# Kernel tuning notes

Measured on AMD Instinct MI355X. Metric: run time of the kernel, lower is better.

Reference implementation:

```python
import jax, jax.numpy as jnp
import numpy as np

V, D, L = 256, 512, 12
B, S = 8, 8192
EPS = 1e-5


def layernorm(x, g, b):
    mu = jnp.mean(x, axis=-1, keepdims=True)
    var = jnp.var(x, axis=-1, keepdims=True)
    return (x - mu) * jax.lax.rsqrt(var + EPS) * g + b


def log_g(x):
    # log of g(x) = x+0.5 if x>=0 else sigmoid(x)
    return jnp.where(x >= 0, jnp.log(jax.nn.relu(x) + 0.5), -jax.nn.softplus(-x))


def heinsen_scan_log(log_coeffs, log_values):
    # h_t = a_t * h_{t-1} + b_t in log-space, parallel over seq (axis=1)
    a_star = jnp.cumsum(log_coeffs, axis=1)
    log_h0_plus_b = jax.lax.cumlogsumexp(log_values - a_star, axis=1)
    return jnp.exp(a_star + log_h0_plus_b)


def min_gru(x, W):
    hg = x @ W                      # [B,S,2D]
    hidden, gate = hg[..., :D], hg[..., D:]
    log_coeffs = -jax.nn.softplus(gate)      # log(1 - z)
    log_z = -jax.nn.softplus(-gate)          # log z
    log_values = log_z + log_g(hidden)
    return heinsen_scan_log(log_coeffs, log_values)


def setup_inputs() -> dict:
    key = jax.random.key(0)
    k0, k1, k2 = jax.random.split(key, 3)
    tokens = jax.random.randint(k0, (B, S), 0, V)
    emb = jax.random.normal(k1, (V, D), dtype=jnp.float32) * 0.02
    # xavier uniform for Linear(D, 2D): fan_in=D, fan_out=2D
    lim = float(np.sqrt(6.0 / (D + 2 * D)))
    W = jax.random.uniform(k2, (L, D, 2 * D), minval=-lim, maxval=lim, dtype=jnp.float32)
    return {
        "tokens": tokens,
        "emb": emb,
        "ln_g": jnp.ones((L, D), jnp.float32),
        "ln_b": jnp.zeros((L, D), jnp.float32),
        "W": W,
        "norm_g": jnp.ones((D,), jnp.float32),
        "norm_b": jnp.zeros((D,), jnp.float32),
    }


def reference(tokens, emb, ln_g, ln_b, W, norm_g, norm_b):
    x = emb[tokens]                 # [B,S,D]
    for i in range(L):
        h = layernorm(x, ln_g[i], ln_b[i])
        x = x + min_gru(h, W[i])
    x = layernorm(x, norm_g, norm_b)
    logits = x @ emb.T              # tied lm_head, [B,S,V]
    return logits
```

## Files before the change

### kernel.cpp

```cpp
#include <hip/hip_runtime.h>
#include <stdint.h>

#define D 512
#define VOCAB 256
#define NLAYER 12
#define BB 8
#define SS 8192
#define CH 128
#define SL 64

typedef __bf16 bf16x8 __attribute__((ext_vector_type(8)));
typedef float f32x4 __attribute__((ext_vector_type(4)));
typedef _Float16 half2_t __attribute__((ext_vector_type(2)));

__device__ __forceinline__ unsigned short f2bf(float f) {
  union { float f; uint32_t u; } c; c.f = f;
  uint32_t u = c.u;
  u += 0x7FFFu + ((u >> 16) & 1u);
  return (unsigned short)(u >> 16);
}

__device__ __forceinline__ void st_f32(float* p, float v) { *p = v; }
__device__ __forceinline__ void st_f32(unsigned short* p, float v) { *p = f2bf(v); }

__device__ __forceinline__ float rcpf_(float x) { return __builtin_amdgcn_rcpf(x); }

__device__ __forceinline__ uint32_t pack_fv(float f, float v) {
  union { half2_t h; uint32_t u; } c;
  c.h.x = (_Float16)f;
  c.h.y = (_Float16)v;
  return c.u;
}

__device__ __forceinline__ void unpack_fv(uint32_t u, float& f, float& v) {
  union { uint32_t u; half2_t h; } c; c.u = u;
  f = (float)c.h.x;
  v = (float)c.h.y;
}

__device__ __forceinline__ void gl_lds16(const unsigned short* g, unsigned short* l) {
  __builtin_amdgcn_global_load_lds((const __attribute__((address_space(1))) void*)(const void*)g,
                                   (__attribute__((address_space(3))) void*)(void*)l, 16, 0, 0);
}

__global__ __launch_bounds__(256) void k_gather(const int* __restrict__ toks,
                                                const float* __restrict__ emb,
                                                float* __restrict__ x) {
  int T = blockIdx.x * 256 + threadIdx.x;
  int row = T >> 6, lane = T & 63;
  int tok = toks[row] & (VOCAB - 1);
  const float4* s = (const float4*)(emb + (size_t)tok * D) + lane * 2;
  float4* d = (float4*)(x + (size_t)row * D) + lane * 2;
  d[0] = s[0];
  d[1] = s[1];
}

__global__ __launch_bounds__(256) void k_convW(const float* __restrict__ W,
                                               unsigned short* __restrict__ Wt) {
  __shared__ float tile[32][33];
  int bid = blockIdx.x;
  int l = bid >> 9;
  int rem = bid & 511;
  int kt = rem >> 5, nt = rem & 31;
  int k0 = kt * 32, n0 = nt * 32;
  int tx = threadIdx.x & 31, ty = threadIdx.x >> 5;
  const float* Wl = W + (size_t)l * D * 2 * D;
  for (int i = 0; i < 4; i++) {
    int k = k0 + ty + 8 * i;
    tile[ty + 8 * i][tx] = Wl[(size_t)k * 1024 + n0 + tx];
  }
  __syncthreads();
  unsigned short* Wtl = Wt + (size_t)l * 1024 * D;
  for (int i = 0; i < 4; i++) {
    int n = n0 + ty + 8 * i;
    Wtl[(size_t)n * D + k0 + tx] = f2bf(tile[tx][ty + 8 * i]);
  }
}

__global__ __launch_bounds__(256) void k_fragW(const unsigned short* __restrict__ Wt,
                                               unsigned short* __restrict__ WtF) {
  int t = blockIdx.x * 256 + threadIdx.x;
  int lane = t & 63;
  int tile = t >> 6;
  int l = tile >> 10;
  int rem = tile & 1023;
  int n16 = rem >> 4, kt = rem & 15;
  const unsigned short* src = Wt + (size_t)l * 1024 * 512 +
                              (size_t)(n16 * 16 + (lane & 15)) * 512 + kt * 32 + (lane >> 4) * 8;
  unsigned short* dst = WtF + (size_t)l * 1024 * 512 + ((size_t)tile * 64 + lane) * 8 -
                        (size_t)l * 1024 * 512 + (size_t)l * 1024 * 512;
  *(uint4*)(WtF + (size_t)l * 524288 + ((size_t)rem * 64 + lane) * 8) = *(const uint4*)src;
  (void)dst;
}

__global__ __launch_bounds__(256) void k_convEmb(const float* __restrict__ e,
                                                 unsigned short* __restrict__ o) {
  int t = blockIdx.x * 256 + threadIdx.x;
  const float4* s = (const float4*)e + (size_t)t * 2;
  float4 a = s[0], b = s[1];
  uint32_t w0 = (uint32_t)f2bf(a.x) | ((uint32_t)f2bf(a.y) << 16);
  uint32_t w1 = (uint32_t)f2bf(a.z) | ((uint32_t)f2bf(a.w) << 16);
  uint32_t w2 = (uint32_t)f2bf(b.x) | ((uint32_t)f2bf(b.y) << 16);
  uint32_t w3 = (uint32_t)f2bf(b.z) | ((uint32_t)f2bf(b.w) << 16);
  uint4 r; r.x = w0; r.y = w1; r.z = w2; r.w = w3;
  ((uint4*)o)[t] = r;
}

__global__ __launch_bounds__(256) void k_ln(const float* __restrict__ x,
                                            const float* __restrict__ g,
                                            const float* __restrict__ b,
                                            unsigned short* __restrict__ o) {
  int wv = threadIdx.x >> 6, lane = threadIdx.x & 63;
  size_t row = (size_t)blockIdx.x * 4 + wv;
  const float4* xr = (const float4*)(x + row * D) + lane * 2;
  float4 v0 = xr[0], v1 = xr[1];
  float s = v0.x + v0.y + v0.z + v0.w + v1.x + v1.y + v1.z + v1.w;
  float ss = v0.x * v0.x + v0.y * v0.y + v0.z * v0.z + v0.w * v0.w +
             v1.x * v1.x + v1.y * v1.y + v1.z * v1.z + v1.w * v1.w;
  for (int m = 32; m; m >>= 1) {
    s += __shfl_xor(s, m, 64);
    ss += __shfl_xor(ss, m, 64);
  }
  float mu = s * (1.0f / 512.0f);
  float var = ss * (1.0f / 512.0f) - mu * mu;
  float rstd = rsqrtf(var + 1e-5f);
  const float4* gp = (const float4*)g + lane * 2;
  const float4* bp = (const float4*)b + lane * 2;
  float4 g0 = gp[0], g1 = gp[1], b0 = bp[0], b1 = bp[1];
  uint32_t w0 = (uint32_t)f2bf((v0.x - mu) * rstd * g0.x + b0.x) |
                ((uint32_t)f2bf((v0.y - mu) * rstd * g0.y + b0.y) << 16);
  uint32_t w1 = (uint32_t)f2bf((v0.z - mu) * rstd * g0.z + b0.z) |
                ((uint32_t)f2bf((v0.w - mu) * rstd * g0.w + b0.w) << 16);
  uint32_t w2 = (uint32_t)f2bf((v1.x - mu) * rstd * g1.x + b1.x) |
                ((uint32_t)f2bf((v1.y - mu) * rstd * g1.y + b1.y) << 16);
  uint32_t w3 = (uint32_t)f2bf((v1.z - mu) * rstd * g1.z + b1.z) |
                ((uint32_t)f2bf((v1.w - mu) * rstd * g1.w + b1.w) << 16);
  uint4 r; r.x = w0; r.y = w1; r.z = w2; r.w = w3;
  ((uint4*)(o + row * D))[lane] = r;
}

__global__ __launch_bounds__(256, 2) void k_gemm_act(const unsigned short* __restrict__ A,
                                                     const unsigned short* __restrict__ Bt,
                                                     uint32_t* __restrict__ fv,
                                                     float* __restrict__ P,
                                                     float* __restrict__ Q) {
  __shared__ __align__(16) unsigned short As[64 * 512];
  const int tid = threadIdx.x;
  const int lane = tid & 63;
  const int wave = tid >> 6;
  const int m0 = blockIdx.x * 64;
  const int qm = lane & 15;
  const int hi = lane >> 4;
  for (int j = 0; j < 16; j++) {
    int r = wave * 16 + j;
    int cg = (lane & ~7) | ((lane & 7) ^ (r & 7));
    gl_lds16(A + (size_t)(m0 + r) * 512 + cg * 8, As + r * 512);
  }
  __syncthreads();

  const int b_loc = m0 >> 13;
  const int c_chunk = (m0 & (SS - 1)) >> 6;
  const size_t pq0 = ((size_t)b_loc * CH + c_chunk) * 512;

  for (int np = 0; np < 2; np++) {
    const int c0 = np * 256 + wave * 64;
    const int n16h = (c0 >> 4);
    f32x4 ah[4][4] = {};
    f32x4 ag[4][4] = {};
    bf16x8 bh[2][4], bg[2][4];
    for (int j = 0; j < 4; j++) {
      bh[0][j] = *(const bf16x8*)(Bt + (((size_t)(n16h + j) * 16 + 0) * 64 + lane) * 8);
      bg[0][j] = *(const bf16x8*)(Bt + (((size_t)(n16h + j + 32) * 16 + 0) * 64 + lane) * 8);
    }
    for (int kt = 0; kt < 16; kt++) {
      const int cur = kt & 1;
      if (kt < 15) {
        const int nxt = cur ^ 1;
        for (int j = 0; j < 4; j++) {
          bh[nxt][j] = *(const bf16x8*)(Bt + (((size_t)(n16h + j) * 16 + kt + 1) * 64 + lane) * 8);
          bg[nxt][j] = *(const bf16x8*)(Bt + (((size_t)(n16h + j + 32) * 16 + kt + 1) * 64 + lane) * 8);
        }
      }
      bf16x8 af[4];
      for (int i = 0; i < 4; i++) {
        int row = i * 16 + qm;
        int cgd = kt * 4 + hi;
        int cl = (cgd & ~7) | ((cgd & 7) ^ (row & 7));
        af[i] = *(const bf16x8*)(&As[row * 512 + cl * 8]);
      }
      for (int i = 0; i < 4; i++)
        for (int j = 0; j < 4; j++) {
          ah[i][j] = __builtin_amdgcn_mfma_f32_16x16x32_bf16(af[i], bh[cur][j], ah[i][j], 0, 0, 0);
          ag[i][j] = __builtin_amdgcn_mfma_f32_16x16x32_bf16(af[i], bg[cur][j], ag[i][j], 0, 0, 0);
        }
    }
    const int rq = hi * 4;
    for (int j = 0; j < 4; j++) {
      float cp = 1.f, cq = 0.f;
      for (int i = 0; i < 4; i++) {
        float sp = 1.f, sq = 0.f;
        for (int r = 0; r < 4; r++) {
          float h = ah[i][j][r];
          float g = ag[i][j][r];
          float e = __expf(g);
          float f = rcpf_(1.0f + e);
          float sg = 1.0f - f;
          float gf = h >= 0.0f ? h + 0.5f : rcpf_(1.0f + __expf(-h));
          float v = sg * gf;
          int rowg = m0 + i * 16 + rq + r;
          fv[(size_t)rowg * 512 + c0 + j * 16 + qm] = pack_fv(f, v);
          sp *= f;
          sq = sq * f + v;
        }
        float op = __shfl_xor(sp, 16), oq = __shfl_xor(sq, 16);
        float tp = sp * op;
        float tq = (lane & 16) ? (oq * sp + sq) : (sq * op + oq);
        op = __shfl_xor(tp, 32); oq = __shfl_xor(tq, 32);
        sp = tp * op;
        sq = (lane & 32) ? (oq * tp + tq) : (tq * op + oq);
        cq = cq * sp + sq;
        cp = cp * sp;
      }
      if (hi == 0) {
        P[pq0 + c0 + j * 16 + qm] = cp;
        Q[pq0 + c0 + j * 16 + qm] = cq;
      }
    }
  }
}

__global__ __launch_bounds__(256) void k_gemm(const unsigned short* __restrict__ A,
                                              const unsigned short* __restrict__ Bt,
                                              float* __restrict__ C, int N, int MT) {
  __shared__ __align__(16) unsigned short As[128 * 64];
  __shared__ __align__(16) unsigned short Bs[128 * 64];
  const int tid = threadIdx.x;
  const int lane = tid & 63;
  const int wave = tid >> 6;
  const int bid = blockIdx.x;
  const int mt = bid % MT;
  const int nt = bid / MT;
  const int m0 = mt * 128, n0 = nt * 128;
  const int wr = (wave >> 1) * 64;
  const int wc = (wave & 1) * 64;
  const int lrow = lane >> 3;
  const int lcs = ((lane & 7) ^ lrow) * 8;
  const unsigned short* Ag = A + (size_t)(m0 + wave * 32 + lrow) * 512 + lcs;
  const unsigned short* Bg = Bt + (size_t)(n0 + wave * 32 + lrow) * 512 + lcs;
  unsigned short* Al = As + wave * 32 * 64;
  unsigned short* Bl = Bs + wave * 32 * 64;
  const int qm = lane & 15;
  const int hi = lane >> 4;
  f32x4 acc[4][4] = {};
  for (int k0 = 0; k0 < 512; k0 += 64) {
    for (int j = 0; j < 4; j++) gl_lds16(Ag + k0 + (size_t)j * 8 * 512, Al + j * 512);
    for (int j = 0; j < 4; j++) gl_lds16(Bg + k0 + (size_t)j * 8 * 512, Bl + j * 512);
    __syncthreads();
    for (int ks = 0; ks < 2; ks++) {
      const int sw = ((ks * 4 + hi) ^ (qm & 7)) * 8;
      bf16x8 af[4], bfr[4];
      for (int i = 0; i < 4; i++) {
        af[i] = *(const bf16x8*)(&As[(wr + i * 16 + qm) * 64 + sw]);
        bfr[i] = *(const bf16x8*)(&Bs[(wc + i * 16 + qm) * 64 + sw]);
      }
      for (int i = 0; i < 4; i++)
        for (int j = 0; j < 4; j++)
          acc[i][j] = __builtin_amdgcn_mfma_f32_16x16x32_bf16(af[i], bfr[j], acc[i][j], 0, 0, 0);
    }
    __syncthreads();
  }
  const int col = lane & 15;
  const int rq = (lane >> 4) * 4;
  for (int i = 0; i < 4; i++)
    for (int j = 0; j < 4; j++)
      for (int r = 0; r < 4; r++)
        C[(size_t)(m0 + wr + i * 16 + rq + r) * N + (n0 + wc + j * 16 + col)] = acc[i][j][r];
}

__global__ __launch_bounds__(256) void k_scan2(const float* __restrict__ P,
                                               const float* __restrict__ Q,
                                               float* __restrict__ Hs) {
  int T = blockIdx.x * 256 + threadIdx.x;
  int d = T & 511;
  int b = T >> 9;
  float h = 0.f;
  for (int c = 0; c < CH; c++) {
    size_t i = ((size_t)b * CH + c) * 512 + d;
    Hs[i] = h;
    h = P[i] * h + Q[i];
  }
}

__global__ __launch_bounds__(256) void k_scan3(const uint32_t* __restrict__ fv,
                                               const float* __restrict__ Hs,
                                               float* __restrict__ x) {
  int T = blockIdx.x * 256 + threadIdx.x;
  int d = T & 511;
  int bc = T >> 9;
  int c = bc & (CH - 1);
  int b = bc >> 7;
  const uint32_t* base = fv + ((size_t)b * SS + c * SL) * 512 + d;
  float* xb = x + ((size_t)b * SS + c * SL) * 512 + d;
  float h = Hs[T];
  for (int s = 0; s < SL; s++) {
    float f, v;
    unpack_fv(base[(size_t)s * 512], f, v);
    h = f * h + v;
    xb[(size_t)s * 512] += h;
  }
}

extern "C" void kernel_launch(void* const* d_in, const int* in_sizes, int n_in,
                              void* d_out, int out_size, void* d_ws, size_t ws_size,
                              hipStream_t stream) {
  const int* toks = (const int*)d_in[0];
  const float* emb = (const float*)d_in[1];
  const float* ln_g = (const float*)d_in[2];
  const float* ln_b = (const float*)d_in[3];
  const float* W = (const float*)d_in[4];
  const float* norm_g = (const float*)d_in[5];
  const float* norm_b = (const float*)d_in[6];
  float* out = (float*)d_out;

  const int gbs[4] = {8, 4, 2, 1};
  int GB = 1;
  for (int i = 0; i < 4; i++) {
    size_t MGv = (size_t)gbs[i] * SS;
    size_t need = MGv * 5120 + 2 * 12582912 + 262144 + (size_t)gbs[i] * 786432;
    if (need <= ws_size) { GB = gbs[i]; break; }
  }
  const int MG = GB * SS;
  const int MT128 = MG / 128;

  char* p = (char*)d_ws;
  float* x = (float*)p;                     p += (size_t)MG * 2048;
  uint32_t* fv = (uint32_t*)p;              p += (size_t)MG * 2048;
  unsigned short* hbf = (unsigned short*)p; p += (size_t)MG * 1024;
  unsigned short* Wtrow = (unsigned short*)p; p += 12582912;
  unsigned short* WtF = (unsigned short*)p;   p += 12582912;
  unsigned short* ebf = (unsigned short*)p;   p += 262144;
  float* P = (float*)p;                     p += (size_t)GB * 262144;
  float* Q = (float*)p;                     p += (size_t)GB * 262144;
  float* Hs = (float*)p;

  k_convW<<<NLAYER * 512, 256, 0, stream>>>(W, Wtrow);
  k_fragW<<<NLAYER * 1024 * 64 / 256, 256, 0, stream>>>(Wtrow, WtF);
  k_convEmb<<<64, 256, 0, stream>>>(emb, ebf);

  for (int g = 0; g < BB / GB; g++) {
    const int* tg = toks + (size_t)g * MG;
    float* outg = out + (size_t)g * MG * VOCAB;

    k_gather<<<MG / 4, 256, 0, stream>>>(tg, emb, x);
    for (int l = 0; l < NLAYER; l++) {
      k_ln<<<MG / 4, 256, 0, stream>>>(x, ln_g + l * D, ln_b + l * D, hbf);
      k_gemm_act<<<MG / 64, 256, 0, stream>>>(hbf, WtF + (size_t)l * 524288, fv, P, Q);
      k_scan2<<<GB * 2, 256, 0, stream>>>(P, Q, Hs);
      k_scan3<<<GB * CH * 2, 256, 0, stream>>>(fv, Hs, x);
    }
    k_ln<<<MG / 4, 256, 0, stream>>>(x, norm_g, norm_b, hbf);
    k_gemm<<<2 * MT128, 256, 0, stream>>>(hbf, ebf, outg, VOCAB, MT128);
  }
}
```

Before: 3.135 ms.

## Fuse layernorm into embedding gather and scan epilogue, dropping separate LN kernels

Layernorm is folded into the embedding gather for layer 0. For later layers it moves into the tail of k_scan3, which now runs one 512-thread block per 64-row chunk and normalizes those rows with the next layer's (or the final) gamma/beta after a block barrier. This removes the standalone k_ln launches and the extra pass over the fp32 residual stream that each of them needed. The cost is a barrier and a re-read of rows the same block just wrote, which are likely cache-resident. It also changes the scan's block shape and occupancy.

Measured after the change: 3.019 ms. 3.7% less time.

```diff
diff --git a/kernel.cpp b/kernel.cpp
--- a/kernel.cpp
+++ b/kernel.cpp
@@ -20,9 +20,6 @@
   return (unsigned short)(u >> 16);
 }
 
-__device__ __forceinline__ void st_f32(float* p, float v) { *p = v; }
-__device__ __forceinline__ void st_f32(unsigned short* p, float v) { *p = f2bf(v); }
-
 __device__ __forceinline__ float rcpf_(float x) { return __builtin_amdgcn_rcpf(x); }
 
 __device__ __forceinline__ uint32_t pack_fv(float f, float v) {
@@ -45,83 +42,26 @@
 
 __global__ __launch_bounds__(256) void k_gather(const int* __restrict__ toks,
                                                 const float* __restrict__ emb,
-                                                float* __restrict__ x) {
+                                                const float* __restrict__ g,
+                                                const float* __restrict__ b,
+                                                float* __restrict__ x,
+                                                unsigned short* __restrict__ o) {
   int T = blockIdx.x * 256 + threadIdx.x;
   int row = T >> 6, lane = T & 63;
   int tok = toks[row] & (VOCAB - 1);
   const float4* s = (const float4*)(emb + (size_t)tok * D) + lane * 2;
+  float4 v0 = s[0], v1 = s[1];
   float4* d = (float4*)(x + (size_t)row * D) + lane * 2;
-  d[0] = s[0];
-  d[1] = s[1];
-}
-
-__global__ __launch_bounds__(256) void k_convW(const float* __restrict__ W,
-                                               unsigned short* __restrict__ Wt) {
-  __shared__ float tile[32][33];
-  int bid = blockIdx.x;
-  int l = bid >> 9;
-  int rem = bid & 511;
-  int kt = rem >> 5, nt = rem & 31;
-  int k0 = kt * 32, n0 = nt * 32;
-  int tx = threadIdx.x & 31, ty = threadIdx.x >> 5;
-  const float* Wl = W + (size_t)l * D * 2 * D;
-  for (int i = 0; i < 4; i++) {
-    int k = k0 + ty + 8 * i;
-    tile[ty + 8 * i][tx] = Wl[(size_t)k * 1024 + n0 + tx];
-  }
-  __syncthreads();
-  unsigned short* Wtl = Wt + (size_t)l * 1024 * D;
-  for (int i = 0; i < 4; i++) {
-    int n = n0 + ty + 8 * i;
-    Wtl[(size_t)n * D + k0 + tx] = f2bf(tile[tx][ty + 8 * i]);
-  }
-}
-
-__global__ __launch_bounds__(256) void k_fragW(const unsigned short* __restrict__ Wt,
-                                               unsigned short* __restrict__ WtF) {
-  int t = blockIdx.x * 256 + threadIdx.x;
-  int lane = t & 63;
-  int tile = t >> 6;
-  int l = tile >> 10;
-  int rem = tile & 1023;
-  int n16 = rem >> 4, kt = rem & 15;
-  const unsigned short* src = Wt + (size_t)l * 1024 * 512 +
-                              (size_t)(n16 * 16 + (lane & 15)) * 512 + kt * 32 + (lane >> 4) * 8;
-  unsigned short* dst = WtF + (size_t)l * 1024 * 512 + ((size_t)tile * 64 + lane) * 8 -
-                        (size_t)l * 1024 * 512 + (size_t)l * 1024 * 512;
-  *(uint4*)(WtF + (size_t)l * 524288 + ((size_t)rem * 64 + lane) * 8) = *(const uint4*)src;
-  (void)dst;
-}
-
-__global__ __launch_bounds__(256) void k_convEmb(const float* __restrict__ e,
-                                                 unsigned short* __restrict__ o) {
-  int t = blockIdx.x * 256 + threadIdx.x;
-  const float4* s = (const float4*)e + (size_t)t * 2;
-  float4 a = s[0], b = s[1];
-  uint32_t w0 = (uint32_t)f2bf(a.x) | ((uint32_t)f2bf(a.y) << 16);
-  uint32_t w1 = (uint32_t)f2bf(a.z) | ((uint32_t)f2bf(a.w) << 16);
-  uint32_t w2 = (uint32_t)f2bf(b.x) | ((uint32_t)f2bf(b.y) << 16);
-  uint32_t w3 = (uint32_t)f2bf(b.z) | ((uint32_t)f2bf(b.w) << 16);
-  uint4 r; r.x = w0; r.y = w1; r.z = w2; r.w = w3;
-  ((uint4*)o)[t] = r;
-}
-
-__global__ __launch_bounds__(256) void k_ln(const float* __restrict__ x,
-                                            const float* __restrict__ g,
-                                            const float* __restrict__ b,
-                                            unsigned short* __restrict__ o) {
-  int wv = threadIdx.x >> 6, lane = threadIdx.x & 63;
-  size_t row = (size_t)blockIdx.x * 4 + wv;
-  const float4* xr = (const float4*)(x + row * D) + lane * 2;
-  float4 v0 = xr[0], v1 = xr[1];
-  float s = v0.x + v0.y + v0.z + v0.w + v1.x + v1.y + v1.z + v1.w;
+  d[0] = v0;
+  d[1] = v1;
+  float sm = v0.x + v0.y + v0.z + v0.w + v1.x + v1.y + v1.z + v1.w;
   float ss = v0.x * v0.x + v0.y * v0.y + v0.z * v0.z + v0.w * v0.w +
              v1.x * v1.x + v1.y * v1.y + v1.z * v1.z + v1.w * v1.w;
   for (int m = 32; m; m >>= 1) {
-    s += __shfl_xor(s, m, 64);
+    sm += __shfl_xor(sm, m, 64);
     ss += __shfl_xor(ss, m, 64);
   }
-  float mu = s * (1.0f / 512.0f);
+  float mu = sm * (1.0f / 512.0f);
   float var = ss * (1.0f / 512.0f) - mu * mu;
   float rstd = rsqrtf(var + 1e-5f);
   const float4* gp = (const float4*)g + lane * 2;
@@ -136,7 +76,55 @@
   uint32_t w3 = (uint32_t)f2bf((v1.z - mu) * rstd * g1.z + b1.z) |
                 ((uint32_t)f2bf((v1.w - mu) * rstd * g1.w + b1.w) << 16);
   uint4 r; r.x = w0; r.y = w1; r.z = w2; r.w = w3;
-  ((uint4*)(o + row * D))[lane] = r;
+  ((uint4*)(o + (size_t)row * D))[lane] = r;
+}
+
+__global__ __launch_bounds__(256) void k_convW(const float* __restrict__ W,
+                                               unsigned short* __restrict__ Wt) {
+  __shared__ float tile[32][33];
+  int bid = blockIdx.x;
+  int l = bid >> 9;
+  int rem = bid & 511;
+  int kt = rem >> 5, nt = rem & 31;
+  int k0 = kt * 32, n0 = nt * 32;
+  int tx = threadIdx.x & 31, ty = threadIdx.x >> 5;
+  const float* Wl = W + (size_t)l * D * 2 * D;
+  for (int i = 0; i < 4; i++) {
+    int k = k0 + ty + 8 * i;
+    tile[ty + 8 * i][tx] = Wl[(size_t)k * 1024 + n0 + tx];
+  }
+  __syncthreads();
+  unsigned short* Wtl = Wt + (size_t)l * 1024 * D;
+  for (int i = 0; i < 4; i++) {
+    int n = n0 + ty + 8 * i;
+    Wtl[(size_t)n * D + k0 + tx] = f2bf(tile[tx][ty + 8 * i]);
+  }
+}
+
+__global__ __launch_bounds__(256) void k_fragW(const unsigned short* __restrict__ Wt,
+                                               unsigned short* __restrict__ WtF) {
+  int t = blockIdx.x * 256 + threadIdx.x;
+  int lane = t & 63;
+  int tile = t >> 6;
+  int l = tile >> 10;
+  int rem = tile & 1023;
+  int n16 = rem >> 4, kt = rem & 15;
+  const unsigned short* src = Wt + (size_t)l * 1024 * 512 +
+                              (size_t)(n16 * 16 + (lane & 15)) * 512 + kt * 32 + (lane >> 4) * 8;
+  *(uint4*)(WtF + (size_t)l * 524288 + ((size_t)rem * 64 + lane) * 8) = *(const uint4*)src;
+}
+
+__global__ __launch_bounds__(256) void k_convEmb(const float* __restrict__ e,
+                                                 unsigned short* __restrict__ o) {
+  int t = blockIdx.x * 256 + threadIdx.x;
+  const float4* s = (const float4*)e + (size_t)t * 2;
+  float4 a = s[0], b = s[1];
+  uint32_t w0 = (uint32_t)f2bf(a.x) | ((uint32_t)f2bf(a.y) << 16);
+  uint32_t w1 = (uint32_t)f2bf(a.z) | ((uint32_t)f2bf(a.w) << 16);
+  uint32_t w2 = (uint32_t)f2bf(b.x) | ((uint32_t)f2bf(b.y) << 16);
+  uint32_t w3 = (uint32_t)f2bf(b.z) | ((uint32_t)f2bf(b.w) << 16);
+  uint4 r; r.x = w0; r.y = w1; r.z = w2; r.w = w3;
+  ((uint4*)o)[t] = r;
 }
 
 __global__ __launch_bounds__(256, 2) void k_gemm_act(const unsigned short* __restrict__ A,
@@ -291,22 +279,57 @@
   }
 }
 
-__global__ __launch_bounds__(256) void k_scan3(const uint32_t* __restrict__ fv,
+__global__ __launch_bounds__(512) void k_scan3(const uint32_t* __restrict__ fv,
                                                const float* __restrict__ Hs,
-                                               float* __restrict__ x) {
-  int T = blockIdx.x * 256 + threadIdx.x;
-  int d = T & 511;
-  int bc = T >> 9;
-  int c = bc & (CH - 1);
-  int b = bc >> 7;
-  const uint32_t* base = fv + ((size_t)b * SS + c * SL) * 512 + d;
-  float* xb = x + ((size_t)b * SS + c * SL) * 512 + d;
-  float h = Hs[T];
+                                               float* __restrict__ x,
+                                               const float* __restrict__ g,
+                                               const float* __restrict__ b,
+                                               unsigned short* __restrict__ o) {
+  const int d = threadIdx.x;
+  const int bc = blockIdx.x;
+  const int c = bc & (CH - 1);
+  const int bb = bc >> 7;
+  const size_t row0 = ((size_t)bb * SS + (size_t)c * SL);
+  const uint32_t* base = fv + row0 * 512 + d;
+  float* xb = x + row0 * 512 + d;
+  float h = Hs[(size_t)bc * 512 + d];
   for (int s = 0; s < SL; s++) {
     float f, v;
     unpack_fv(base[(size_t)s * 512], f, v);
     h = f * h + v;
     xb[(size_t)s * 512] += h;
+  }
+  __syncthreads();
+
+  const int wv = threadIdx.x >> 6, lane = threadIdx.x & 63;
+  const float4* gp = (const float4*)g + lane * 2;
+  const float4* bp = (const float4*)b + lane * 2;
+  float4 g0 = gp[0], g1 = gp[1], b0 = bp[0], b1 = bp[1];
+  const float* xr0 = x + row0 * 512;
+  for (int rr = 0; rr < 8; rr++) {
+    int r = wv * 8 + rr;
+    const float4* xr = (const float4*)(xr0 + (size_t)r * 512) + lane * 2;
+    float4 v0 = xr[0], v1 = xr[1];
+    float sm = v0.x + v0.y + v0.z + v0.w + v1.x + v1.y + v1.z + v1.w;
+    float ss = v0.x * v0.x + v0.y * v0.y + v0.z * v0.z + v0.w * v0.w +
+               v1.x * v1.x + v1.y * v1.y + v1.z * v1.z + v1.w * v1.w;
+    for (int m = 32; m; m >>= 1) {
+      sm += __shfl_xor(sm, m, 64);
+      ss += __shfl_xor(ss, m, 64);
+    }
+    float mu = sm * (1.0f / 512.0f);
+    float var = ss * (1.0f / 512.0f) - mu * mu;
+    float rstd = rsqrtf(var + 1e-5f);
+    uint32_t w0 = (uint32_t)f2bf((v0.x - mu) * rstd * g0.x + b0.x) |
+                  ((uint32_t)f2bf((v0.y - mu) * rstd * g0.y + b0.y) << 16);
+    uint32_t w1 = (uint32_t)f2bf((v0.z - mu) * rstd * g0.z + b0.z) |
+                  ((uint32_t)f2bf((v0.w - mu) * rstd * g0.w + b0.w) << 16);
+    uint32_t w2 = (uint32_t)f2bf((v1.x - mu) * rstd * g1.x + b1.x) |
+                  ((uint32_t)f2bf((v1.y - mu) * rstd * g1.y + b1.y) << 16);
+    uint32_t w3 = (uint32_t)f2bf((v1.z - mu) * rstd * g1.z + b1.z) |
+                  ((uint32_t)f2bf((v1.w - mu) * rstd * g1.w + b1.w) << 16);
+    uint4 rr4; rr4.x = w0; rr4.y = w1; rr4.z = w2; rr4.w = w3;
+    ((uint4*)(o + (row0 + r) * 512))[lane] = rr4;
   }
 }
 
@@ -351,14 +374,14 @@
     const int* tg = toks + (size_t)g * MG;
     float* outg = out + (size_t)g * MG * VOCAB;
 
-    k_gather<<<MG / 4, 256, 0, stream>>>(tg, emb, x);
+    k_gather<<<MG / 4, 256, 0, stream>>>(tg, emb, ln_g, ln_b, x, hbf);
     for (int l = 0; l < NLAYER; l++) {
-      k_ln<<<MG / 4, 256, 0, stream>>>(x, ln_g + l * D, ln_b + l * D, hbf);
       k_gemm_act<<<MG / 64, 256, 0, stream>>>(hbf, WtF + (size_t)l * 524288, fv, P, Q);
       k_scan2<<<GB * 2, 256, 0, stream>>>(P, Q, Hs);
-      k_scan3<<<GB * CH * 2, 256, 0, stream>>>(fv, Hs, x);
-    }
-    k_ln<<<MG / 4, 256, 0, stream>>>(x, norm_g, norm_b, hbf);
+      const float* gn = (l < NLAYER - 1) ? (ln_g + (size_t)(l + 1) * D) : norm_g;
+      const float* bn = (l < NLAYER - 1) ? (ln_b + (size_t)(l + 1) * D) : norm_b;
+      k_scan3<<<GB * CH, 512, 0, stream>>>(fv, Hs, x, gn, bn, hbf);
+    }
     k_gemm<<<2 * MT128, 256, 0, stream>>>(hbf, ebf, outg, VOCAB, MT128);
   }
 }
```
